# Kernel tuning notes

Measured on AMD Instinct MI355X. Metric: run time of the kernel, lower is better.

Reference implementation:

```python
import jax, jax.numpy as jnp
import numpy as np

N, D = 200000, 512

def setup_inputs() -> dict:
    key = jax.random.key(0)
    k1, k2, k3 = jax.random.split(key, 3)
    data_in = jax.random.normal(k1, (1, D), dtype=jnp.float32)
    ukb_mat = jax.random.normal(k2, (N, D), dtype=jnp.float32)
    pseudo = jax.random.uniform(k3, (N,), dtype=jnp.float32)
    return {"data_in": data_in, "ukb_mat": ukb_mat, "pseudo": pseudo, "K": 3}

def reference(data_in, ukb_mat, pseudo, K):
    # L1 distance from the single query to every reference row: [N]
    dist = jnp.sum(jnp.abs(data_in - ukb_mat), axis=1)
    # K smallest distances == top-K of negated distances (partial selection,
    # same indices as tf.argsort(...)[:K] modulo tie order)
    _, top_k_ind = jax.lax.top_k(-dist, K)
    inference_score = jnp.mean(pseudo[top_k_ind])
    return jnp.expand_dims(inference_score, 0)  # shape [1]
```

## Files before the change

### kernel.cpp

```cpp
#include <hip/hip_runtime.h>
#include <float.h>


#define P1_BLOCKS       1024
#define P1_THREADS      256
#define WAVES_PER_BLOCK (P1_THREADS / 64)
#define TOTAL_WAVES     (P1_BLOCKS * WAVES_PER_BLOCK)
#define NUM_PART        (TOTAL_WAVES * 3)
#define DCOLS           512

__device__ __forceinline__ void top3_insert(float s, int r,
                                            float& d0, float& d1, float& d2,
                                            int& i0, int& i1, int& i2) {
    if (s < d2 || (s == d2 && r < i2)) {
        d2 = s; i2 = r;
        if (d2 < d1 || (d2 == d1 && i2 < i1)) {
            float td = d1; d1 = d2; d2 = td;
            int   ti = i1; i1 = i2; i2 = ti;
        }
        if (d1 < d0 || (d1 == d0 && i1 < i0)) {
            float td = d0; d0 = d1; d1 = td;
            int   ti = i0; i0 = i1; i1 = ti;
        }
    }
}

__global__ __launch_bounds__(P1_THREADS) void l1_top3_phase1(
        const float* __restrict__ q, const float* __restrict__ mat,
        float* __restrict__ part_d, int* __restrict__ part_i, int N) {
    const int lane = threadIdx.x & 63;
    const int wave = blockIdx.x * WAVES_PER_BLOCK + (threadIdx.x >> 6);

    const float4 q0 = ((const float4*)q)[lane];
    const float4 q1 = ((const float4*)q)[64 + lane];

    float d0 = FLT_MAX, d1 = FLT_MAX, d2 = FLT_MAX;
    int   i0 = -1, i1 = -1, i2 = -1;

    for (int row = wave; row < N; row += TOTAL_WAVES) {
        const float4* rp = (const float4*)(mat + (size_t)row * DCOLS);
        float4 a = rp[lane];
        float4 b = rp[64 + lane];
        float s = fabsf(a.x - q0.x) + fabsf(a.y - q0.y)
                + fabsf(a.z - q0.z) + fabsf(a.w - q0.w)
                + fabsf(b.x - q1.x) + fabsf(b.y - q1.y)
                + fabsf(b.z - q1.z) + fabsf(b.w - q1.w);
        #pragma unroll
        for (int m = 32; m >= 1; m >>= 1) s += __shfl_xor(s, m, 64);
        top3_insert(s, row, d0, d1, d2, i0, i1, i2);
    }
    if (lane == 0) {
        part_d[wave * 3 + 0] = d0; part_i[wave * 3 + 0] = i0;
        part_d[wave * 3 + 1] = d1; part_i[wave * 3 + 1] = i1;
        part_d[wave * 3 + 2] = d2; part_i[wave * 3 + 2] = i2;
    }
}

__global__ __launch_bounds__(256) void top3_phase2(
        const float* __restrict__ part_d, const int* __restrict__ part_i,
        const float* __restrict__ pseudo, const int* __restrict__ Kp,
        float* __restrict__ out, int num) {
    float d0 = FLT_MAX, d1 = FLT_MAX, d2 = FLT_MAX;
    int   i0 = -1, i1 = -1, i2 = -1;

    for (int j = threadIdx.x; j < num; j += 256)
        top3_insert(part_d[j], part_i[j], d0, d1, d2, i0, i1, i2);

    __shared__ float sd[256 * 3];
    __shared__ int   si[256 * 3];
    sd[threadIdx.x * 3 + 0] = d0; si[threadIdx.x * 3 + 0] = i0;
    sd[threadIdx.x * 3 + 1] = d1; si[threadIdx.x * 3 + 1] = i1;
    sd[threadIdx.x * 3 + 2] = d2; si[threadIdx.x * 3 + 2] = i2;
    __syncthreads();

    if (threadIdx.x < 64) {
        #pragma unroll
        for (int b = 1; b < 4; ++b) {
            int base = (threadIdx.x + b * 64) * 3;
            top3_insert(sd[base + 0], si[base + 0], d0, d1, d2, i0, i1, i2);
            top3_insert(sd[base + 1], si[base + 1], d0, d1, d2, i0, i1, i2);
            top3_insert(sd[base + 2], si[base + 2], d0, d1, d2, i0, i1, i2);
        }
        #pragma unroll
        for (int m = 32; m >= 1; m >>= 1) {
            float pd0 = __shfl_xor(d0, m, 64);
            float pd1 = __shfl_xor(d1, m, 64);
            float pd2 = __shfl_xor(d2, m, 64);
            int   pi0 = __shfl_xor(i0, m, 64);
            int   pi1 = __shfl_xor(i1, m, 64);
            int   pi2 = __shfl_xor(i2, m, 64);
            top3_insert(pd0, pi0, d0, d1, d2, i0, i1, i2);
            top3_insert(pd1, pi1, d0, d1, d2, i0, i1, i2);
            top3_insert(pd2, pi2, d0, d1, d2, i0, i1, i2);
        }
        if (threadIdx.x == 0) {
            int K = Kp[0];
            if (K < 1) K = 1;
            if (K > 3) K = 3;
            float sum = pseudo[i0];
            if (K > 1) sum += pseudo[i1];
            if (K > 2) sum += pseudo[i2];
            out[0] = sum / (float)K;
        }
    }
}

extern "C" void kernel_launch(void* const* d_in, const int* in_sizes, int n_in,
                              void* d_out, int out_size, void* d_ws, size_t ws_size,
                              hipStream_t stream) {
    const float* data_in = (const float*)d_in[0];
    const float* ukb_mat = (const float*)d_in[1];
    const float* pseudo  = (const float*)d_in[2];
    const int*   Kp      = (const int*)d_in[3];
    float*       out     = (float*)d_out;

    const int N = in_sizes[1] / DCOLS;

    float* part_d = (float*)d_ws;
    int*   part_i = (int*)((char*)d_ws + (size_t)NUM_PART * sizeof(float));

    l1_top3_phase1<<<P1_BLOCKS, P1_THREADS, 0, stream>>>(
        data_in, ukb_mat, part_d, part_i, N);
    top3_phase2<<<1, 256, 0, stream>>>(
        part_d, part_i, pseudo, Kp, out, NUM_PART);
}
```

Before: 549.9 us.

## Process four rows per wave and reduce top-3 within block

Each wave now handles four rows per iteration, with 16 lanes per row issuing eight vector loads each through nontemporal loads. This cuts the shuffle reduction depth and raises the loads in flight per lane. Per-wave top-3 lists are merged across row groups and then across waves in shared memory, so each block writes one set of partials and the second kernel scans fewer candidates. This costs extra registers for the query copy and adds a block-level synchronization.

```diff
diff --git a/kernel.cpp b/kernel.cpp
--- a/kernel.cpp
+++ b/kernel.cpp
@@ -6,8 +6,11 @@
 #define P1_THREADS      256
 #define WAVES_PER_BLOCK (P1_THREADS / 64)
 #define TOTAL_WAVES     (P1_BLOCKS * WAVES_PER_BLOCK)
-#define NUM_PART        (TOTAL_WAVES * 3)
+#define ROWS_PER_ITER   (TOTAL_WAVES * 4)
+#define NUM_PART        (P1_BLOCKS * 3)
 #define DCOLS           512
+
+typedef float fx4 __attribute__((ext_vector_type(4)));
 
 __device__ __forceinline__ void top3_insert(float s, int r,
                                             float& d0, float& d1, float& d2,
@@ -29,30 +32,70 @@
         const float* __restrict__ q, const float* __restrict__ mat,
         float* __restrict__ part_d, int* __restrict__ part_i, int N) {
     const int lane = threadIdx.x & 63;
-    const int wave = blockIdx.x * WAVES_PER_BLOCK + (threadIdx.x >> 6);
+    const int sub  = lane & 15;
+    const int grp  = lane >> 4;
+    const int wv   = threadIdx.x >> 6;
+    const int wave = blockIdx.x * WAVES_PER_BLOCK + wv;
 
-    const float4 q0 = ((const float4*)q)[lane];
-    const float4 q1 = ((const float4*)q)[64 + lane];
+    fx4 qf[8];
+    #pragma unroll
+    for (int k = 0; k < 8; ++k) qf[k] = ((const fx4*)q)[sub + 16 * k];
 
     float d0 = FLT_MAX, d1 = FLT_MAX, d2 = FLT_MAX;
     int   i0 = -1, i1 = -1, i2 = -1;
 
-    for (int row = wave; row < N; row += TOTAL_WAVES) {
-        const float4* rp = (const float4*)(mat + (size_t)row * DCOLS);
-        float4 a = rp[lane];
-        float4 b = rp[64 + lane];
-        float s = fabsf(a.x - q0.x) + fabsf(a.y - q0.y)
-                + fabsf(a.z - q0.z) + fabsf(a.w - q0.w)
-                + fabsf(b.x - q1.x) + fabsf(b.y - q1.y)
-                + fabsf(b.z - q1.z) + fabsf(b.w - q1.w);
+    for (int base = wave * 4; base < N; base += ROWS_PER_ITER) {
+        const int row = base + grp;
+        float s;
+        if (row < N) {
+            const fx4* rp = (const fx4*)(mat + (size_t)row * DCOLS);
+            s = 0.0f;
+            #pragma unroll
+            for (int k = 0; k < 8; ++k) {
+                fx4 a = __builtin_nontemporal_load(rp + sub + 16 * k);
+                s += fabsf(a.x - qf[k].x) + fabsf(a.y - qf[k].y)
+                   + fabsf(a.z - qf[k].z) + fabsf(a.w - qf[k].w);
+            }
+        } else {
+            s = FLT_MAX;
+        }
+        s += __shfl_xor(s, 1, 64);
+        s += __shfl_xor(s, 2, 64);
+        s += __shfl_xor(s, 4, 64);
+        s += __shfl_xor(s, 8, 64);
+        if (row < N) top3_insert(s, row, d0, d1, d2, i0, i1, i2);
+    }
+
+    #pragma unroll
+    for (int m = 16; m <= 32; m <<= 1) {
+        float pd0 = __shfl_xor(d0, m, 64);
+        float pd1 = __shfl_xor(d1, m, 64);
+        float pd2 = __shfl_xor(d2, m, 64);
+        int   pi0 = __shfl_xor(i0, m, 64);
+        int   pi1 = __shfl_xor(i1, m, 64);
+        int   pi2 = __shfl_xor(i2, m, 64);
+        top3_insert(pd0, pi0, d0, d1, d2, i0, i1, i2);
+        top3_insert(pd1, pi1, d0, d1, d2, i0, i1, i2);
+        top3_insert(pd2, pi2, d0, d1, d2, i0, i1, i2);
+    }
+
+    __shared__ float swd[WAVES_PER_BLOCK * 3];
+    __shared__ int   swi[WAVES_PER_BLOCK * 3];
+    if (lane == 0) {
+        swd[wv * 3 + 0] = d0; swi[wv * 3 + 0] = i0;
+        swd[wv * 3 + 1] = d1; swi[wv * 3 + 1] = i1;
+        swd[wv * 3 + 2] = d2; swi[wv * 3 + 2] = i2;
+    }
+    __syncthreads();
+    if (threadIdx.x == 0) {
+        float e0 = FLT_MAX, e1 = FLT_MAX, e2 = FLT_MAX;
+        int   j0 = -1, j1 = -1, j2 = -1;
         #pragma unroll
-        for (int m = 32; m >= 1; m >>= 1) s += __shfl_xor(s, m, 64);
-        top3_insert(s, row, d0, d1, d2, i0, i1, i2);
-    }
-    if (lane == 0) {
-        part_d[wave * 3 + 0] = d0; part_i[wave * 3 + 0] = i0;
-        part_d[wave * 3 + 1] = d1; part_i[wave * 3 + 1] = i1;
-        part_d[wave * 3 + 2] = d2; part_i[wave * 3 + 2] = i2;
+        for (int t = 0; t < WAVES_PER_BLOCK * 3; ++t)
+            top3_insert(swd[t], swi[t], e0, e1, e2, j0, j1, j2);
+        part_d[blockIdx.x * 3 + 0] = e0; part_i[blockIdx.x * 3 + 0] = j0;
+        part_d[blockIdx.x * 3 + 1] = e1; part_i[blockIdx.x * 3 + 1] = j1;
+        part_d[blockIdx.x * 3 + 2] = e2; part_i[blockIdx.x * 3 + 2] = j2;
     }
 }
 
```

Result: faster. 512.9 us (-6.7%).
